# Optimization experiments

Hardware: AMD Instinct MI355X
Metric: run time of the kernel (lower is better)

The kernel has to match this reference:

```python
import jax, jax.numpy as jnp
import numpy as np

N = 50000          # num nodes
E = 800000         # num edges (before self-loops)
D = 256            # feature dim for all layers
C = 2              # num classes
SLOPE = 0.2        # GATConv default negative_slope


def setup_inputs() -> dict:
    key = jax.random.key(0)
    ks = jax.random.split(key, 14)
    s = 1.0 / np.sqrt(D)
    inp = {
        "x": jax.random.normal(ks[0], (N, D), dtype=jnp.float32),
        "edge_index": jax.random.randint(ks[1], (2, E), 0, N, dtype=jnp.int64),
        # GAT layer 1 (heads=1): lin weight, att_src, att_dst, bias
        "W1": jax.random.normal(ks[2], (D, D), dtype=jnp.float32) * s,
        "a1s": jax.random.normal(ks[3], (D,), dtype=jnp.float32) * s,
        "a1d": jax.random.normal(ks[4], (D,), dtype=jnp.float32) * s,
        "b1": jnp.zeros((D,), dtype=jnp.float32),
        # GAT layer 2
        "W2": jax.random.normal(ks[5], (D, D), dtype=jnp.float32) * s,
        "a2s": jax.random.normal(ks[6], (D,), dtype=jnp.float32) * s,
        "a2d": jax.random.normal(ks[7], (D,), dtype=jnp.float32) * s,
        "b2": jnp.zeros((D,), dtype=jnp.float32),
        # classifier
        "Wc": jax.random.normal(ks[8], (D, C), dtype=jnp.float32) * s,
        "bc": jnp.zeros((C,), dtype=jnp.float32),
    }
    return inp


def _gat_layer(x, src, dst, W, a_src, a_dst, b):
    """PyG GATConv (heads=1, concat=True) with self-loops already in src/dst."""
    h = x @ W                                   # [N, D] node GEMM
    es = h @ a_src                              # [N] per-node src attention term
    ed = h @ a_dst                              # [N]
    e = jax.nn.leaky_relu(es[src] + ed[dst], SLOPE)   # [E'] per-edge logit
    # segment softmax over incoming edges of each dst node
    m = jax.ops.segment_max(e, dst, num_segments=N)   # [N]
    ex = jnp.exp(e - m[dst])
    den = jax.ops.segment_sum(ex, dst, num_segments=N)
    alpha = ex / den[dst]                       # [E']
    # weighted scatter-aggregate of source features
    out = jax.ops.segment_sum(alpha[:, None] * h[src], dst, num_segments=N)
    return out + b


def reference(x, edge_index, W1, a1s, a1d, b1, W2, a2s, a2d, b2, Wc, bc):
    loops = jnp.arange(N, dtype=edge_index.dtype)
    src = jnp.concatenate([edge_index[0], loops])   # add_self_loops=True
    dst = jnp.concatenate([edge_index[1], loops])
    h = jax.nn.relu(_gat_layer(x, src, dst, W1, a1s, a1d, b1))
    h = jax.nn.relu(_gat_layer(h, src, dst, W2, a2s, a2d, b2))
    logits = h @ Wc + bc                        # [N, C]
    return jax.nn.log_softmax(logits, axis=1)
```

## Files before the change

### kernel.cpp

```cpp
#include <hip/hip_runtime.h>
#include <math.h>

#define N_NODES 50000
#define N_EDGES 800000
#define EP (N_EDGES + N_NODES)
#define D 256
#define SLOPE 0.2f
#define CAP 64
#define TWG 512
#define CASTG 12500
#define SCATG 3321

typedef __attribute__((ext_vector_type(8))) short short8;
typedef __attribute__((ext_vector_type(4))) float f32x4;
typedef const __attribute__((address_space(1))) unsigned int* as1_u32;
typedef __attribute__((address_space(3))) unsigned int* as3_u32;

__device__ __forceinline__ unsigned short f2b(float f) {
    unsigned u = __float_as_uint(f);
    unsigned r = (u + 0x7FFFu + ((u >> 16) & 1u)) >> 16;
    return (unsigned short)r;
}
__device__ __forceinline__ float uas(unsigned u) { return __uint_as_float(u); }
__device__ __forceinline__ void g2lds16(const void* g, void* l) {
    __builtin_amdgcn_global_load_lds((as1_u32)g, (as3_u32)l, 16, 0, 0);
}


__global__ __launch_bounds__(256) void prep(const int* __restrict__ ei,
                                            const float* __restrict__ W1,
                                            const float* __restrict__ W2,
                                            const float* __restrict__ x,
                                            unsigned short* __restrict__ Wt1,
                                            unsigned short* __restrict__ Wt2,
                                            unsigned short* __restrict__ xb,
                                            int* __restrict__ cnt,
                                            int* __restrict__ srcC) {
    __shared__ float t[16][17];
    int bid = blockIdx.x;
    if (bid < TWG) {
        int t2 = bid;
        const float* W = (t2 < 256) ? W1 : W2;
        unsigned short* Wt = (t2 < 256) ? Wt1 : Wt2;
        int tile = t2 & 255;
        int bx = (tile & 15) * 16, by = (tile >> 4) * 16;
        int lx = threadIdx.x & 15, ly = threadIdx.x >> 4;
        t[ly][lx] = W[(bx + ly) * D + by + lx];
        __syncthreads();
        Wt[(by + ly) * D + bx + lx] = f2b(t[lx][ly]);
    } else if (bid < TWG + CASTG) {
        int i = (bid - TWG) * 256 + threadIdx.x;
        float4 v = ((const float4*)x)[i];
        ushort4 o;
        o.x = f2b(v.x); o.y = f2b(v.y); o.z = f2b(v.z); o.w = f2b(v.w);
        ((ushort4*)xb)[i] = o;
    } else {
        int k = (bid - TWG - CASTG) * 256 + threadIdx.x;
        if (k >= EP) return;
        int s, d;
        if (k < N_EDGES) { s = ei[k]; d = ei[N_EDGES + k]; }
        else             { s = d = k - N_EDGES; }
        int slot = atomicAdd(&cnt[d], 1);
        if (slot < CAP) srcC[(d << 6) + slot] = s;
    }
}


__global__ __launch_bounds__(256) void gemm_bf16(const short* __restrict__ A,
                                                 const short* __restrict__ Wt,
                                                 unsigned short* __restrict__ C,
                                                 const float* __restrict__ avs,
                                                 const float* __restrict__ avd,
                                                 float* __restrict__ es,
                                                 float* __restrict__ ed) {
    __shared__ short lA[128 * 64];
    __shared__ short lB[128 * 64];
    int bid = blockIdx.x;
    int cb, y;
    if (bid < 768) { int g2 = bid >> 4, r = bid & 15; y = g2 * 8 + (r & 7); cb = r >> 3; }
    else           { int t = bid - 768; y = 384 + (t >> 1); cb = t & 1; }
    int row0 = y << 7;
    int col0 = cb << 7;
    int tid = threadIdx.x, wave = tid >> 6, lane = tid & 63;
    int q = lane >> 4, m = lane & 15;
    int lr = lane >> 3;
    int kseg = (lane & 7) ^ lr;

    f32x4 acc[2][8] = {};
    for (int kc = 0; kc < 4; ++kc) {
        if (kc) __syncthreads();
#pragma unroll
        for (int it = 0; it < 4; ++it) {
            int rl = wave * 32 + it * 8;
            int gr = row0 + rl + lr;
            if (gr >= N_NODES) gr = N_NODES - 1;
            g2lds16(A + (((size_t)gr) << 8) + kc * 64 + kseg * 8, &lA[rl * 64]);
            int gc = col0 + rl + lr;
            g2lds16(Wt + (((size_t)gc) << 8) + kc * 64 + kseg * 8, &lB[rl * 64]);
        }
        __syncthreads();
#pragma unroll
        for (int ks = 0; ks < 2; ++ks) {
            int sw = ((ks * 4 + q) ^ (m & 7)) * 8;
            short8 a0 = *(const short8*)&lA[(wave * 32 + m) * 64 + sw];
            short8 a1 = *(const short8*)&lA[(wave * 32 + 16 + m) * 64 + sw];
#pragma unroll
            for (int ct = 0; ct < 8; ++ct) {
                short8 bf = *(const short8*)&lB[(ct * 16 + m) * 64 + sw];
                acc[0][ct] = __builtin_amdgcn_mfma_f32_16x16x32_bf16(a0, bf, acc[0][ct], 0, 0, 0);
                acc[1][ct] = __builtin_amdgcn_mfma_f32_16x16x32_bf16(a1, bf, acc[1][ct], 0, 0, 0);
            }
        }
    }

    float asv[8], adv[8];
#pragma unroll
    for (int ct = 0; ct < 8; ++ct) {
        asv[ct] = avs[col0 + ct * 16 + m];
        adv[ct] = avd[col0 + ct * 16 + m];
    }
    int rbase = row0 + wave * 32;
#pragma unroll
    for (int rt = 0; rt < 2; ++rt) {
        float ps[4] = {0.f, 0.f, 0.f, 0.f};
        float pd[4] = {0.f, 0.f, 0.f, 0.f};
#pragma unroll
        for (int ct = 0; ct < 8; ++ct)
#pragma unroll
            for (int rr = 0; rr < 4; ++rr) {
                float v = acc[rt][ct][rr];
                int row = rbase + rt * 16 + q * 4 + rr;
                if (row < N_NODES)
                    C[(((size_t)row) << 8) + col0 + ct * 16 + m] = f2b(v);
                ps[rr] += v * asv[ct];
                pd[rr] += v * adv[ct];
            }
#pragma unroll
        for (int rr = 0; rr < 4; ++rr) {
#pragma unroll
            for (int off = 1; off < 16; off <<= 1) {
                ps[rr] += __shfl_xor(ps[rr], off);
                pd[rr] += __shfl_xor(pd[rr], off);
            }
        }
        if (m == 0) {
#pragma unroll
            for (int rr = 0; rr < 4; ++rr) {
                int row = rbase + rt * 16 + q * 4 + rr;
                if (row < N_NODES) {
                    atomicAdd(&es[row], ps[rr]);
                    atomicAdd(&ed[row], pd[rr]);
                }
            }
        }
    }
}


template<int CLS>
__global__ __launch_bounds__(256) void aggregate(const unsigned short* __restrict__ h,
                                                 const float* __restrict__ es,
                                                 const float* __restrict__ ed,
                                                 const int* __restrict__ cntv,
                                                 const int* __restrict__ srcC,
                                                 const float* __restrict__ bias,
                                                 unsigned short* __restrict__ outg,
                                                 const float* __restrict__ Wc,
                                                 const float* __restrict__ bc,
                                                 float* __restrict__ out) {
    __shared__ float wbuf[4][64];
    __shared__ int   sbuf[4][64];
    int wv = threadIdx.x >> 6;
    int node = blockIdx.x * 4 + wv;
    if (node >= N_NODES) return;
    int lane = threadIdx.x & 63;
    int lane32 = lane & 31, half = lane >> 5;
    size_t fo = (size_t)lane32 * 8;
    int cnt = cntv[node];
    if (cnt > CAP) cnt = CAP;
    float edn = ed[node];

    int s = node;
    float w = 0.f;
    if (lane < cnt) {
        s = srcC[(node << 6) + lane];
        float e = es[s] + edn;
        e = e > 0.f ? e : SLOPE * e;
        w = __expf(fminf(e, 80.f));
    }
    wbuf[wv][lane] = w;
    sbuf[wv][lane] = s;
    float den = w;
    float accf[8] = {};

#pragma unroll 8
    for (int jj = 0; jj < cnt; jj += 2) {
        int idx = jj + half;
        float wj = wbuf[wv][idx];
        int sj = sbuf[wv][idx];
        uint4 u = *(const uint4*)&h[(((size_t)sj) << 8) + fo];
        accf[0] += wj * uas(u.x << 16);
        accf[1] += wj * uas(u.x & 0xffff0000u);
        accf[2] += wj * uas(u.y << 16);
        accf[3] += wj * uas(u.y & 0xffff0000u);
        accf[4] += wj * uas(u.z << 16);
        accf[5] += wj * uas(u.z & 0xffff0000u);
        accf[6] += wj * uas(u.w << 16);
        accf[7] += wj * uas(u.w & 0xffff0000u);
    }
    for (int off = 32; off; off >>= 1) den += __shfl_xor(den, off);
#pragma unroll
    for (int i = 0; i < 8; ++i) accf[i] += __shfl_xor(accf[i], 32);

    float inv = 1.f / den;
    float4 b0 = *(const float4*)&bias[fo];
    float4 b1 = *(const float4*)&bias[fo + 4];
    float r[8];
    r[0] = fmaxf(accf[0] * inv + b0.x, 0.f);
    r[1] = fmaxf(accf[1] * inv + b0.y, 0.f);
    r[2] = fmaxf(accf[2] * inv + b0.z, 0.f);
    r[3] = fmaxf(accf[3] * inv + b0.w, 0.f);
    r[4] = fmaxf(accf[4] * inv + b1.x, 0.f);
    r[5] = fmaxf(accf[5] * inv + b1.y, 0.f);
    r[6] = fmaxf(accf[6] * inv + b1.z, 0.f);
    r[7] = fmaxf(accf[7] * inv + b1.w, 0.f);

    if (!CLS) {
        if (half == 0) {
            short8 o;
#pragma unroll
            for (int i = 0; i < 8; ++i) o[i] = (short)f2b(r[i]);
            *(short8*)&outg[(((size_t)node) << 8) + fo] = o;
        }
    } else {
        float l0 = 0.f, l1 = 0.f;
#pragma unroll
        for (int f2 = 0; f2 < 4; ++f2) {
            float4 wc = *(const float4*)&Wc[fo * 2 + f2 * 4];
            l0 += r[f2 * 2] * wc.x + r[f2 * 2 + 1] * wc.z;
            l1 += r[f2 * 2] * wc.y + r[f2 * 2 + 1] * wc.w;
        }
#pragma unroll
        for (int off = 1; off < 32; off <<= 1) {
            l0 += __shfl_xor(l0, off);
            l1 += __shfl_xor(l1, off);
        }
        if (lane == 0) {
            l0 += bc[0];
            l1 += bc[1];
            float mx = fmaxf(l0, l1);
            float z = logf(__expf(l0 - mx) + __expf(l1 - mx));
            out[node * 2 + 0] = l0 - mx - z;
            out[node * 2 + 1] = l1 - mx - z;
        }
    }
}


extern "C" void kernel_launch(void* const* d_in, const int* in_sizes, int n_in,
                              void* d_out, int out_size, void* d_ws, size_t ws_size,
                              hipStream_t stream) {
    const float* x   = (const float*)d_in[0];
    const int*   ei  = (const int*)d_in[1];
    const float* W1  = (const float*)d_in[2];
    const float* a1s = (const float*)d_in[3];
    const float* a1d = (const float*)d_in[4];
    const float* b1  = (const float*)d_in[5];
    const float* W2  = (const float*)d_in[6];
    const float* a2s = (const float*)d_in[7];
    const float* a2d = (const float*)d_in[8];
    const float* b2  = (const float*)d_in[9];
    const float* Wc  = (const float*)d_in[10];
    const float* bc  = (const float*)d_in[11];
    float* out = (float*)d_out;

    char* p = (char*)d_ws;
    unsigned short* xb  = (unsigned short*)p; p += (size_t)N_NODES * D * 2;
    unsigned short* h   = (unsigned short*)p; p += (size_t)N_NODES * D * 2;
    unsigned short* g   = (unsigned short*)p; p += (size_t)N_NODES * D * 2;
    unsigned short* Wt1 = (unsigned short*)p; p += (size_t)D * D * 2;
    unsigned short* Wt2 = (unsigned short*)p; p += (size_t)D * D * 2;
    int* srcC = (int*)p;    p += (size_t)N_NODES * CAP * 4;
    int*   cnt = (int*)p;   p += (size_t)N_NODES * 4;
    float* es1 = (float*)p; p += (size_t)N_NODES * 4;
    float* ed1 = (float*)p; p += (size_t)N_NODES * 4;
    float* es2 = (float*)p; p += (size_t)N_NODES * 4;
    float* ed2 = (float*)p; p += (size_t)N_NODES * 4;

    hipMemsetAsync(cnt, 0, (size_t)5 * N_NODES * 4, stream);

    dim3 b256(256);
    int ngrid = (N_NODES + 3) / 4;

    prep<<<TWG + CASTG + SCATG, b256, 0, stream>>>(ei, W1, W2, x, Wt1, Wt2, xb, cnt, srcC);

    gemm_bf16<<<782, b256, 0, stream>>>((const short*)xb, (const short*)Wt1, h,
                                        a1s, a1d, es1, ed1);
    aggregate<0><<<ngrid, b256, 0, stream>>>(h, es1, ed1, cnt, srcC, b1, g,
                                             nullptr, nullptr, nullptr);
    gemm_bf16<<<782, b256, 0, stream>>>((const short*)g, (const short*)Wt2, h,
                                        a2s, a2d, es2, ed2);
    aggregate<1><<<ngrid, b256, 0, stream>>>(h, es2, ed2, cnt, srcC, b2, nullptr,
                                             Wc, bc, out);
}
```

Baseline: 342.6 us.

## Split GAT aggregation into edge-weight, feature-slab aggregate, and classifier kernels

```diff
diff --git a/kernel.cpp b/kernel.cpp
--- a/kernel.cpp
+++ b/kernel.cpp
@@ -7,9 +7,9 @@
 #define D 256
 #define SLOPE 0.2f
 #define CAP 64
+#define SCATG 3321
 #define TWG 512
 #define CASTG 12500
-#define SCATG 3321
 
 typedef __attribute__((ext_vector_type(8))) short short8;
 typedef __attribute__((ext_vector_type(4))) float f32x4;
@@ -38,8 +38,16 @@
                                             int* __restrict__ srcC) {
     __shared__ float t[16][17];
     int bid = blockIdx.x;
-    if (bid < TWG) {
-        int t2 = bid;
+    if (bid < SCATG) {
+        int k = bid * 256 + threadIdx.x;
+        if (k >= EP) return;
+        int s, d;
+        if (k < N_EDGES) { s = ei[k]; d = ei[N_EDGES + k]; }
+        else             { s = d = k - N_EDGES; }
+        int slot = atomicAdd(&cnt[d], 1);
+        if (slot < CAP) srcC[(d << 6) + slot] = s;
+    } else if (bid < SCATG + TWG) {
+        int t2 = bid - SCATG;
         const float* W = (t2 < 256) ? W1 : W2;
         unsigned short* Wt = (t2 < 256) ? Wt1 : Wt2;
         int tile = t2 & 255;
@@ -48,20 +56,12 @@
         t[ly][lx] = W[(bx + ly) * D + by + lx];
         __syncthreads();
         Wt[(by + ly) * D + bx + lx] = f2b(t[lx][ly]);
-    } else if (bid < TWG + CASTG) {
-        int i = (bid - TWG) * 256 + threadIdx.x;
+    } else {
+        int i = (bid - SCATG - TWG) * 256 + threadIdx.x;
         float4 v = ((const float4*)x)[i];
         ushort4 o;
         o.x = f2b(v.x); o.y = f2b(v.y); o.z = f2b(v.z); o.w = f2b(v.w);
         ((ushort4*)xb)[i] = o;
-    } else {
-        int k = (bid - TWG - CASTG) * 256 + threadIdx.x;
-        if (k >= EP) return;
-        int s, d;
-        if (k < N_EDGES) { s = ei[k]; d = ei[N_EDGES + k]; }
-        else             { s = d = k - N_EDGES; }
-        int slot = atomicAdd(&cnt[d], 1);
-        if (slot < CAP) srcC[(d << 6) + slot] = s;
     }
 }
 
@@ -71,8 +71,8 @@
                                                  unsigned short* __restrict__ C,
                                                  const float* __restrict__ avs,
                                                  const float* __restrict__ avd,
-                                                 float* __restrict__ es,
-                                                 float* __restrict__ ed) {
+                                                 float* __restrict__ esp,
+                                                 float* __restrict__ edp) {
     __shared__ short lA[128 * 64];
     __shared__ short lB[128 * 64];
     int bid = blockIdx.x;
@@ -119,6 +119,8 @@
         asv[ct] = avs[col0 + ct * 16 + m];
         adv[ct] = avd[col0 + ct * 16 + m];
     }
+    float* esw = esp + (cb ? N_NODES : 0);
+    float* edw = edp + (cb ? N_NODES : 0);
     int rbase = row0 + wave * 32;
 #pragma unroll
     for (int rt = 0; rt < 2; ++rt) {
@@ -148,8 +150,8 @@
             for (int rr = 0; rr < 4; ++rr) {
                 int row = rbase + rt * 16 + q * 4 + rr;
                 if (row < N_NODES) {
-                    atomicAdd(&es[row], ps[rr]);
-                    atomicAdd(&ed[row], pd[rr]);
+                    esw[row] = ps[rr];
+                    edw[row] = pd[rr];
                 }
             }
         }
@@ -157,102 +159,108 @@
 }
 
 
-template<int CLS>
-__global__ __launch_bounds__(256) void aggregate(const unsigned short* __restrict__ h,
-                                                 const float* __restrict__ es,
-                                                 const float* __restrict__ ed,
-                                                 const int* __restrict__ cntv,
-                                                 const int* __restrict__ srcC,
-                                                 const float* __restrict__ bias,
-                                                 unsigned short* __restrict__ outg,
-                                                 const float* __restrict__ Wc,
-                                                 const float* __restrict__ bc,
-                                                 float* __restrict__ out) {
-    __shared__ float wbuf[4][64];
-    __shared__ int   sbuf[4][64];
-    int wv = threadIdx.x >> 6;
-    int node = blockIdx.x * 4 + wv;
-    if (node >= N_NODES) return;
+__global__ __launch_bounds__(256) void edgew(const float* __restrict__ esp,
+                                             const float* __restrict__ edp,
+                                             const int* __restrict__ cntv,
+                                             const int* __restrict__ srcC,
+                                             int2* __restrict__ pw) {
+    int node = blockIdx.x * 4 + (threadIdx.x >> 6);
     int lane = threadIdx.x & 63;
-    int lane32 = lane & 31, half = lane >> 5;
-    size_t fo = (size_t)lane32 * 8;
-    int cnt = cntv[node];
-    if (cnt > CAP) cnt = CAP;
-    float edn = ed[node];
-
-    int s = node;
-    float w = 0.f;
-    if (lane < cnt) {
-        s = srcC[(node << 6) + lane];
-        float e = es[s] + edn;
-        e = e > 0.f ? e : SLOPE * e;
-        w = __expf(fminf(e, 80.f));
-    }
-    wbuf[wv][lane] = w;
-    sbuf[wv][lane] = s;
-    float den = w;
-    float accf[8] = {};
-
-#pragma unroll 8
-    for (int jj = 0; jj < cnt; jj += 2) {
-        int idx = jj + half;
-        float wj = wbuf[wv][idx];
-        int sj = sbuf[wv][idx];
-        uint4 u = *(const uint4*)&h[(((size_t)sj) << 8) + fo];
-        accf[0] += wj * uas(u.x << 16);
-        accf[1] += wj * uas(u.x & 0xffff0000u);
-        accf[2] += wj * uas(u.y << 16);
-        accf[3] += wj * uas(u.y & 0xffff0000u);
-        accf[4] += wj * uas(u.z << 16);
-        accf[5] += wj * uas(u.z & 0xffff0000u);
-        accf[6] += wj * uas(u.w << 16);
-        accf[7] += wj * uas(u.w & 0xffff0000u);
-    }
-    for (int off = 32; off; off >>= 1) den += __shfl_xor(den, off);
-#pragma unroll
-    for (int i = 0; i < 8; ++i) accf[i] += __shfl_xor(accf[i], 32);
-
-    float inv = 1.f / den;
-    float4 b0 = *(const float4*)&bias[fo];
-    float4 b1 = *(const float4*)&bias[fo + 4];
-    float r[8];
-    r[0] = fmaxf(accf[0] * inv + b0.x, 0.f);
-    r[1] = fmaxf(accf[1] * inv + b0.y, 0.f);
-    r[2] = fmaxf(accf[2] * inv + b0.z, 0.f);
-    r[3] = fmaxf(accf[3] * inv + b0.w, 0.f);
-    r[4] = fmaxf(accf[4] * inv + b1.x, 0.f);
-    r[5] = fmaxf(accf[5] * inv + b1.y, 0.f);
-    r[6] = fmaxf(accf[6] * inv + b1.z, 0.f);
-    r[7] = fmaxf(accf[7] * inv + b1.w, 0.f);
-
-    if (!CLS) {
-        if (half == 0) {
+    int c = cntv[node];
+    if (c > CAP) c = CAP;
+    if (lane >= c) return;
+    float edn = edp[node] + edp[N_NODES + node];
+    int s = srcC[(node << 6) + lane];
+    float e = esp[s] + esp[N_NODES + s] + edn;
+    e = e > 0.f ? e : SLOPE * e;
+    float w = __expf(fminf(e, 80.f));
+    pw[(node << 6) + lane] = make_int2(s, __float_as_int(w));
+}
+
+
+__global__ __launch_bounds__(256) void aggS(const unsigned short* __restrict__ h,
+                                            const int* __restrict__ cntv,
+                                            const int2* __restrict__ pw,
+                                            const float* __restrict__ bias,
+                                            unsigned short* __restrict__ outg) {
+    int slab = blockIdx.x & 7;
+    int ng = blockIdx.x >> 3;
+    int wv = threadIdx.x >> 6, lane = threadIdx.x & 63;
+    int eg = lane >> 2, fq = lane & 3;
+    int fbase = slab * 32 + fq * 8;
+    float4 bv0 = *(const float4*)&bias[fbase];
+    float4 bv1 = *(const float4*)&bias[fbase + 4];
+
+#pragma unroll
+    for (int rep = 0; rep < 2; ++rep) {
+        int node = ng * 8 + wv * 2 + rep;
+        int c = cntv[node];
+        if (c > CAP) c = CAP;
+        int2 v = pw[(node << 6) + lane];
+        float wl = (lane < c) ? __int_as_float(v.y) : 0.f;
+        float den = wl;
+        for (int off = 32; off; off >>= 1) den += __shfl_xor(den, off);
+        float acc[8] = {};
+        for (int base = 0; base < c; base += 16) {
+            int e = base + eg;
+            float we = __shfl(wl, e);
+            int se = __shfl(v.x, e);
+            if (e >= c) se = node;
+            uint4 u = *(const uint4*)&h[(((size_t)se) << 8) + fbase];
+            acc[0] += we * uas(u.x << 16);
+            acc[1] += we * uas(u.x & 0xffff0000u);
+            acc[2] += we * uas(u.y << 16);
+            acc[3] += we * uas(u.y & 0xffff0000u);
+            acc[4] += we * uas(u.z << 16);
+            acc[5] += we * uas(u.z & 0xffff0000u);
+            acc[6] += we * uas(u.w << 16);
+            acc[7] += we * uas(u.w & 0xffff0000u);
+        }
+#pragma unroll
+        for (int off = 4; off < 64; off <<= 1)
+#pragma unroll
+            for (int i = 0; i < 8; ++i) acc[i] += __shfl_xor(acc[i], off);
+        if (eg == 0) {
+            float inv = 1.f / den;
             short8 o;
-#pragma unroll
-            for (int i = 0; i < 8; ++i) o[i] = (short)f2b(r[i]);
-            *(short8*)&outg[(((size_t)node) << 8) + fo] = o;
-        }
-    } else {
-        float l0 = 0.f, l1 = 0.f;
-#pragma unroll
-        for (int f2 = 0; f2 < 4; ++f2) {
-            float4 wc = *(const float4*)&Wc[fo * 2 + f2 * 4];
-            l0 += r[f2 * 2] * wc.x + r[f2 * 2 + 1] * wc.z;
-            l1 += r[f2 * 2] * wc.y + r[f2 * 2 + 1] * wc.w;
-        }
-#pragma unroll
-        for (int off = 1; off < 32; off <<= 1) {
-            l0 += __shfl_xor(l0, off);
-            l1 += __shfl_xor(l1, off);
-        }
-        if (lane == 0) {
-            l0 += bc[0];
-            l1 += bc[1];
-            float mx = fmaxf(l0, l1);
-            float z = logf(__expf(l0 - mx) + __expf(l1 - mx));
-            out[node * 2 + 0] = l0 - mx - z;
-            out[node * 2 + 1] = l1 - mx - z;
-        }
+            o[0] = (short)f2b(fmaxf(acc[0] * inv + bv0.x, 0.f));
+            o[1] = (short)f2b(fmaxf(acc[1] * inv + bv0.y, 0.f));
+            o[2] = (short)f2b(fmaxf(acc[2] * inv + bv0.z, 0.f));
+            o[3] = (short)f2b(fmaxf(acc[3] * inv + bv0.w, 0.f));
+            o[4] = (short)f2b(fmaxf(acc[4] * inv + bv1.x, 0.f));
+            o[5] = (short)f2b(fmaxf(acc[5] * inv + bv1.y, 0.f));
+            o[6] = (short)f2b(fmaxf(acc[6] * inv + bv1.z, 0.f));
+            o[7] = (short)f2b(fmaxf(acc[7] * inv + bv1.w, 0.f));
+            *(short8*)&outg[(((size_t)node) << 8) + fbase] = o;
+        }
+    }
+}
+
+
+__global__ __launch_bounds__(256) void classifier(const unsigned short* __restrict__ g,
+                                                  const float* __restrict__ Wc,
+                                                  const float* __restrict__ bc,
+                                                  float* __restrict__ out) {
+    int node = blockIdx.x * 4 + (threadIdx.x >> 6);
+    int lane = threadIdx.x & 63;
+    uint2 u = *(const uint2*)&g[(((size_t)node) << 8) + lane * 4];
+    float h0 = uas(u.x << 16), h1 = uas(u.x & 0xffff0000u);
+    float h2 = uas(u.y << 16), h3 = uas(u.y & 0xffff0000u);
+    float4 w01 = *(const float4*)&Wc[lane * 8];
+    float4 w23 = *(const float4*)&Wc[lane * 8 + 4];
+    float l0 = h0 * w01.x + h1 * w01.z + h2 * w23.x + h3 * w23.z;
+    float l1 = h0 * w01.y + h1 * w01.w + h2 * w23.y + h3 * w23.w;
+    for (int off = 32; off; off >>= 1) {
+        l0 += __shfl_xor(l0, off);
+        l1 += __shfl_xor(l1, off);
+    }
+    if (lane == 0) {
+        l0 += bc[0];
+        l1 += bc[1];
+        float mx = fmaxf(l0, l1);
+        float z = logf(__expf(l0 - mx) + __expf(l1 - mx));
+        out[node * 2 + 0] = l0 - mx - z;
+        out[node * 2 + 1] = l1 - mx - z;
     }
 }
 
@@ -280,26 +288,25 @@
     unsigned short* g   = (unsigned short*)p; p += (size_t)N_NODES * D * 2;
     unsigned short* Wt1 = (unsigned short*)p; p += (size_t)D * D * 2;
     unsigned short* Wt2 = (unsigned short*)p; p += (size_t)D * D * 2;
-    int* srcC = (int*)p;    p += (size_t)N_NODES * CAP * 4;
-    int*   cnt = (int*)p;   p += (size_t)N_NODES * 4;
-    float* es1 = (float*)p; p += (size_t)N_NODES * 4;
-    float* ed1 = (float*)p; p += (size_t)N_NODES * 4;
-    float* es2 = (float*)p; p += (size_t)N_NODES * 4;
-    float* ed2 = (float*)p; p += (size_t)N_NODES * 4;
-
-    hipMemsetAsync(cnt, 0, (size_t)5 * N_NODES * 4, stream);
+    int*  srcC = (int*)p;  p += (size_t)N_NODES * CAP * 4;
+    int2* pw   = (int2*)p; p += (size_t)N_NODES * CAP * 8;
+    float* esp = (float*)p; p += (size_t)2 * N_NODES * 4;
+    float* edp = (float*)p; p += (size_t)2 * N_NODES * 4;
+    int*  cnt  = (int*)p;  p += (size_t)N_NODES * 4;
+
+    hipMemsetAsync(cnt, 0, (size_t)N_NODES * 4, stream);
 
     dim3 b256(256);
-    int ngrid = (N_NODES + 3) / 4;
-
-    prep<<<TWG + CASTG + SCATG, b256, 0, stream>>>(ei, W1, W2, x, Wt1, Wt2, xb, cnt, srcC);
+
+    prep<<<SCATG + TWG + CASTG, b256, 0, stream>>>(ei, W1, W2, x, Wt1, Wt2, xb, cnt, srcC);
 
     gemm_bf16<<<782, b256, 0, stream>>>((const short*)xb, (const short*)Wt1, h,
-                                        a1s, a1d, es1, ed1);
-    aggregate<0><<<ngrid, b256, 0, stream>>>(h, es1, ed1, cnt, srcC, b1, g,
-                                             nullptr, nullptr, nullptr);
+                                        a1s, a1d, esp, edp);
+    edgew<<<12500, b256, 0, stream>>>(esp, edp, cnt, srcC, pw);
+    aggS<<<50000, b256, 0, stream>>>(h, cnt, pw, b1, g);
     gemm_bf16<<<782, b256, 0, stream>>>((const short*)g, (const short*)Wt2, h,
-                                        a2s, a2d, es2, ed2);
-    aggregate<1><<<ngrid, b256, 0, stream>>>(h, es2, ed2, cnt, srcC, b2, nullptr,
-                                             Wc, bc, out);
-}
+                                        a2s, a2d, esp, edp);
+    edgew<<<12500, b256, 0, stream>>>(esp, edp, cnt, srcC, pw);
+    aggS<<<50000, b256, 0, stream>>>(h, cnt, pw, b2, xb);
+    classifier<<<12500, b256, 0, stream>>>(xb, Wc, bc, out);
+}
```

Measured after the change: 595.8 us. 1.74x slower.

## Replace per-node atomic edge bucketing with two-pass binned CSR sort, stage GEMM stores

Applied to the files above, without the earlier changes.

```diff
diff --git a/kernel.cpp b/kernel.cpp
--- a/kernel.cpp
+++ b/kernel.cpp
@@ -6,10 +6,13 @@
 #define EP (N_EDGES + N_NODES)
 #define D 256
 #define SLOPE 0.2f
-#define CAP 64
+#define NBIN 196
+#define BINB 6144
+#define SORTA 208
+#define SAE 4096
 #define TWG 512
 #define CASTG 12500
-#define SCATG 3321
+#define GEMMB 782
 
 typedef __attribute__((ext_vector_type(8))) short short8;
 typedef __attribute__((ext_vector_type(4))) float f32x4;
@@ -27,19 +30,44 @@
 }
 
 
-__global__ __launch_bounds__(256) void prep(const int* __restrict__ ei,
-                                            const float* __restrict__ W1,
-                                            const float* __restrict__ W2,
-                                            const float* __restrict__ x,
-                                            unsigned short* __restrict__ Wt1,
-                                            unsigned short* __restrict__ Wt2,
-                                            unsigned short* __restrict__ xb,
-                                            int* __restrict__ cnt,
-                                            int* __restrict__ srcC) {
+__global__ __launch_bounds__(256) void prep0(const int* __restrict__ ei,
+                                             const float* __restrict__ W1,
+                                             const float* __restrict__ W2,
+                                             const float* __restrict__ x,
+                                             unsigned short* __restrict__ Wt1,
+                                             unsigned short* __restrict__ Wt2,
+                                             unsigned short* __restrict__ xb,
+                                             int* __restrict__ binCnt,
+                                             int* __restrict__ coarse) {
     __shared__ float t[16][17];
+    __shared__ int hist[NBIN], base[NBIN], lrk[NBIN];
     int bid = blockIdx.x;
-    if (bid < TWG) {
-        int t2 = bid;
+    if (bid < SORTA) {
+        int e0 = bid * SAE;
+        for (int i = threadIdx.x; i < NBIN; i += 256) { hist[i] = 0; lrk[i] = 0; }
+        __syncthreads();
+        for (int i = threadIdx.x; i < SAE; i += 256) {
+            int k = e0 + i;
+            if (k >= EP) break;
+            int d = (k < N_EDGES) ? ei[N_EDGES + k] : (k - N_EDGES);
+            atomicAdd(&hist[d >> 8], 1);
+        }
+        __syncthreads();
+        for (int i = threadIdx.x; i < NBIN; i += 256)
+            if (hist[i]) base[i] = atomicAdd(&binCnt[i], hist[i]);
+        __syncthreads();
+        for (int i = threadIdx.x; i < SAE; i += 256) {
+            int k = e0 + i;
+            if (k >= EP) break;
+            int s, d;
+            if (k < N_EDGES) { s = ei[k]; d = ei[N_EDGES + k]; }
+            else             { s = d = k - N_EDGES; }
+            int b = d >> 8;
+            int r = base[b] + atomicAdd(&lrk[b], 1);
+            if (r < BINB) coarse[b * BINB + r] = s | ((d & 255) << 16);
+        }
+    } else if (bid < SORTA + TWG) {
+        int t2 = bid - SORTA;
         const float* W = (t2 < 256) ? W1 : W2;
         unsigned short* Wt = (t2 < 256) ? Wt1 : Wt2;
         int tile = t2 & 255;
@@ -48,21 +76,60 @@
         t[ly][lx] = W[(bx + ly) * D + by + lx];
         __syncthreads();
         Wt[(by + ly) * D + bx + lx] = f2b(t[lx][ly]);
-    } else if (bid < TWG + CASTG) {
-        int i = (bid - TWG) * 256 + threadIdx.x;
+    } else {
+        int i = (bid - SORTA - TWG) * 256 + threadIdx.x;
         float4 v = ((const float4*)x)[i];
         ushort4 o;
         o.x = f2b(v.x); o.y = f2b(v.y); o.z = f2b(v.z); o.w = f2b(v.w);
         ((ushort4*)xb)[i] = o;
-    } else {
-        int k = (bid - TWG - CASTG) * 256 + threadIdx.x;
-        if (k >= EP) return;
-        int s, d;
-        if (k < N_EDGES) { s = ei[k]; d = ei[N_EDGES + k]; }
-        else             { s = d = k - N_EDGES; }
-        int slot = atomicAdd(&cnt[d], 1);
-        if (slot < CAP) srcC[(d << 6) + slot] = s;
-    }
+    }
+}
+
+
+__global__ __launch_bounds__(1024) void sortB(const int* __restrict__ coarse,
+                                              const int* __restrict__ binCnt,
+                                              int* __restrict__ srcC,
+                                              int2* __restrict__ rpc) {
+    __shared__ int h[256], off[256], h2[256];
+    __shared__ int ssrc[BINB];
+    int bin = blockIdx.x, tid = threadIdx.x;
+    int cnt = binCnt[bin];
+    if (cnt > BINB) cnt = BINB;
+    if (tid < 256) { h[tid] = 0; h2[tid] = 0; }
+    __syncthreads();
+    int vv[6]; int nv = 0;
+#pragma unroll
+    for (int it = 0; it < 6; ++it) {
+        int i = it * 1024 + tid;
+        if (i < cnt) {
+            int v = coarse[bin * BINB + i];
+            vv[nv++] = v;
+            atomicAdd(&h[v >> 16], 1);
+        }
+    }
+    __syncthreads();
+    if (tid < 256) off[tid] = h[tid];
+    __syncthreads();
+    for (int o = 1; o < 256; o <<= 1) {
+        int tv = (tid < 256 && tid >= o) ? off[tid - o] : 0;
+        __syncthreads();
+        if (tid < 256) off[tid] += tv;
+        __syncthreads();
+    }
+    for (int j = 0; j < nv; ++j) {
+        int ld = vv[j] >> 16;
+        int pos = off[ld] - h[ld] + atomicAdd(&h2[ld], 1);
+        ssrc[pos] = vv[j] & 0xffff;
+    }
+    __syncthreads();
+#pragma unroll
+    for (int it = 0; it < 6; ++it) {
+        int i = it * 1024 + tid;
+        if (i < cnt) srcC[bin * BINB + i] = ssrc[i];
+    }
+    int node = bin * 256 + tid;
+    if (tid < 256 && node < N_NODES)
+        rpc[node] = make_int2(bin * BINB + off[tid] - h[tid], h[tid]);
 }
 
 
@@ -71,10 +138,11 @@
                                                  unsigned short* __restrict__ C,
                                                  const float* __restrict__ avs,
                                                  const float* __restrict__ avd,
-                                                 float* __restrict__ es,
-                                                 float* __restrict__ ed) {
-    __shared__ short lA[128 * 64];
-    __shared__ short lB[128 * 64];
+                                                 float* __restrict__ esp,
+                                                 float* __restrict__ edp) {
+    __shared__ short sbuf[128 * 132];
+    short* lA = sbuf;
+    short* lB = sbuf + 128 * 64;
     int bid = blockIdx.x;
     int cb, y;
     if (bid < 768) { int g2 = bid >> 4, r = bid & 15; y = g2 * 8 + (r & 7); cb = r >> 3; }
@@ -119,6 +187,8 @@
         asv[ct] = avs[col0 + ct * 16 + m];
         adv[ct] = avd[col0 + ct * 16 + m];
     }
+    float* esw = esp + (cb ? N_NODES : 0);
+    float* edw = edp + (cb ? N_NODES : 0);
     int rbase = row0 + wave * 32;
 #pragma unroll
     for (int rt = 0; rt < 2; ++rt) {
@@ -129,9 +199,6 @@
 #pragma unroll
             for (int rr = 0; rr < 4; ++rr) {
                 float v = acc[rt][ct][rr];
-                int row = rbase + rt * 16 + q * 4 + rr;
-                if (row < N_NODES)
-                    C[(((size_t)row) << 8) + col0 + ct * 16 + m] = f2b(v);
                 ps[rr] += v * asv[ct];
                 pd[rr] += v * adv[ct];
             }
@@ -148,20 +215,40 @@
             for (int rr = 0; rr < 4; ++rr) {
                 int row = rbase + rt * 16 + q * 4 + rr;
                 if (row < N_NODES) {
-                    atomicAdd(&es[row], ps[rr]);
-                    atomicAdd(&ed[row], pd[rr]);
+                    esw[row] = ps[rr];
+                    edw[row] = pd[rr];
                 }
             }
         }
+    }
+
+    __syncthreads();
+#pragma unroll
+    for (int rt = 0; rt < 2; ++rt)
+#pragma unroll
+        for (int ct = 0; ct < 8; ++ct)
+#pragma unroll
+            for (int rr = 0; rr < 4; ++rr) {
+                int lrow = wave * 32 + rt * 16 + q * 4 + rr;
+                sbuf[lrow * 132 + ct * 16 + m] = (short)f2b(acc[rt][ct][rr]);
+            }
+    __syncthreads();
+#pragma unroll
+    for (int it = 0; it < 8; ++it) {
+        int idx = it * 256 + tid;
+        int lrow = idx >> 4, cg = idx & 15;
+        int row = row0 + lrow;
+        if (row < N_NODES)
+            *(short8*)&C[(((size_t)row) << 8) + col0 + cg * 8] = *(const short8*)&sbuf[lrow * 132 + cg * 8];
     }
 }
 
 
 template<int CLS>
 __global__ __launch_bounds__(256) void aggregate(const unsigned short* __restrict__ h,
-                                                 const float* __restrict__ es,
-                                                 const float* __restrict__ ed,
-                                                 const int* __restrict__ cntv,
+                                                 const float* __restrict__ esp,
+                                                 const float* __restrict__ edp,
+                                                 const int2* __restrict__ rpc,
                                                  const int* __restrict__ srcC,
                                                  const float* __restrict__ bias,
                                                  unsigned short* __restrict__ outg,
@@ -176,15 +263,16 @@
     int lane = threadIdx.x & 63;
     int lane32 = lane & 31, half = lane >> 5;
     size_t fo = (size_t)lane32 * 8;
-    int cnt = cntv[node];
-    if (cnt > CAP) cnt = CAP;
-    float edn = ed[node];
+    int2 rc = rpc[node];
+    int start = rc.x;
+    int cnt = rc.y > 64 ? 64 : rc.y;
+    float edn = edp[node] + edp[N_NODES + node];
 
     int s = node;
     float w = 0.f;
     if (lane < cnt) {
-        s = srcC[(node << 6) + lane];
-        float e = es[s] + edn;
+        s = srcC[start + lane];
+        float e = esp[s] + esp[N_NODES + s] + edn;
         e = e > 0.f ? e : SLOPE * e;
         w = __expf(fminf(e, 80.f));
     }
@@ -280,26 +368,27 @@
     unsigned short* g   = (unsigned short*)p; p += (size_t)N_NODES * D * 2;
     unsigned short* Wt1 = (unsigned short*)p; p += (size_t)D * D * 2;
     unsigned short* Wt2 = (unsigned short*)p; p += (size_t)D * D * 2;
-    int* srcC = (int*)p;    p += (size_t)N_NODES * CAP * 4;
-    int*   cnt = (int*)p;   p += (size_t)N_NODES * 4;
-    float* es1 = (float*)p; p += (size_t)N_NODES * 4;
-    float* ed1 = (float*)p; p += (size_t)N_NODES * 4;
-    float* es2 = (float*)p; p += (size_t)N_NODES * 4;
-    float* ed2 = (float*)p; p += (size_t)N_NODES * 4;
-
-    hipMemsetAsync(cnt, 0, (size_t)5 * N_NODES * 4, stream);
+    int*  coarse = (int*)p;  p += (size_t)NBIN * BINB * 4;
+    int*  srcC   = (int*)p;  p += (size_t)NBIN * BINB * 4;
+    int2* rpc    = (int2*)p; p += (size_t)N_NODES * 8;
+    float* esp   = (float*)p; p += (size_t)2 * N_NODES * 4;
+    float* edp   = (float*)p; p += (size_t)2 * N_NODES * 4;
+    int*  binCnt = (int*)p;  p += (size_t)NBIN * 4;
+
+    hipMemsetAsync(binCnt, 0, (size_t)NBIN * 4, stream);
 
     dim3 b256(256);
     int ngrid = (N_NODES + 3) / 4;
 
-    prep<<<TWG + CASTG + SCATG, b256, 0, stream>>>(ei, W1, W2, x, Wt1, Wt2, xb, cnt, srcC);
-
-    gemm_bf16<<<782, b256, 0, stream>>>((const short*)xb, (const short*)Wt1, h,
-                                        a1s, a1d, es1, ed1);
-    aggregate<0><<<ngrid, b256, 0, stream>>>(h, es1, ed1, cnt, srcC, b1, g,
+    prep0<<<SORTA + TWG + CASTG, b256, 0, stream>>>(ei, W1, W2, x, Wt1, Wt2, xb, binCnt, coarse);
+    sortB<<<NBIN, 1024, 0, stream>>>(coarse, binCnt, srcC, rpc);
+
+    gemm_bf16<<<GEMMB, b256, 0, stream>>>((const short*)xb, (const short*)Wt1, h,
+                                          a1s, a1d, esp, edp);
+    aggregate<0><<<ngrid, b256, 0, stream>>>(h, esp, edp, rpc, srcC, b1, g,
                                              nullptr, nullptr, nullptr);
-    gemm_bf16<<<782, b256, 0, stream>>>((const short*)g, (const short*)Wt2, h,
-                                        a2s, a2d, es2, ed2);
-    aggregate<1><<<ngrid, b256, 0, stream>>>(h, es2, ed2, cnt, srcC, b2, nullptr,
+    gemm_bf16<<<GEMMB, b256, 0, stream>>>((const short*)g, (const short*)Wt2, h,
+                                          a2s, a2d, esp, edp);
+    aggregate<1><<<ngrid, b256, 0, stream>>>(h, esp, edp, rpc, srcC, b2, nullptr,
                                              Wc, bc, out);
 }
```

Measured after the change: 308.6 us. 9.9% less time.
